# Performance work log

Measured on AMD Instinct MI355X. Metric: run time of the kernel, lower is better.

The kernel has to match this reference:

```python
import jax, jax.numpy as jnp
import numpy as np

N = 100000   # nodes per node type
E = 1000000  # edges per edge type
C = 128      # channels
H = 4        # num_heads
D = C // H   # head_dim


def setup_inputs() -> dict:
    key = jax.random.key(0)
    ks = jax.random.split(key, 16)
    return {
        "x_A": jax.random.normal(ks[0], (N, C), jnp.float32),
        "x_B": jax.random.normal(ks[1], (N, C), jnp.float32),
        "Wq": jax.random.normal(ks[2], (C, C), jnp.float32) * 0.05,
        "bq": jax.random.normal(ks[3], (C,), jnp.float32) * 0.05,
        "Wk": jax.random.normal(ks[4], (C, C), jnp.float32) * 0.05,
        "bk": jax.random.normal(ks[5], (C,), jnp.float32) * 0.05,
        "Wv": jax.random.normal(ks[6], (C, C), jnp.float32) * 0.05,
        "bv": jax.random.normal(ks[7], (C,), jnp.float32) * 0.05,
        "gamma": jnp.ones((C,), jnp.float32),
        "beta": jnp.zeros((C,), jnp.float32),
        "bias_AB": jax.random.normal(ks[8], (1,), jnp.float32),
        "bias_BA": jax.random.normal(ks[9], (1,), jnp.float32),
        "sb_AB": jax.random.normal(ks[10], (E,), jnp.float32),
        "sb_BA": jax.random.normal(ks[11], (E,), jnp.float32),
        "edge_index_AB": jax.random.randint(ks[12], (2, E), 0, N, jnp.int32),
        "edge_index_BA": jax.random.randint(ks[13], (2, E), 0, N, jnp.int32),
    }


def _edge_attention(x_src, x_dst, src, dst, sb, etype_bias, Wq, bq, Wk, bk, Wv, bv):
    """Per-edge-type attention: gather -> score -> dst-segment softmax -> scatter-add."""
    n_dst = x_dst.shape[0]
    Q = (x_dst @ Wq.T + bq).reshape(n_dst, H, D)
    K = (x_src @ Wk.T + bk).reshape(-1, H, D)
    V = (x_src @ Wv.T + bv).reshape(-1, H, D)
    # [E, H] per-edge scores
    scores = jnp.einsum('ehd,ehd->eh', Q[dst], K[src]) / np.float32(np.sqrt(D))
    scores = scores + sb[:, None] + etype_bias  # spatial bias + edge-type bias
    # segment softmax over edges grouped by dst node (numerically stable)
    m = jax.ops.segment_max(scores, dst, num_segments=n_dst)
    ex = jnp.exp(scores - m[dst])
    denom = jax.ops.segment_sum(ex, dst, num_segments=n_dst)
    w = ex / denom[dst]  # [E, H]
    msg = (V[src] * w[:, :, None]).reshape(-1, C)  # [E, C]
    return jax.ops.segment_sum(msg, dst, num_segments=n_dst)  # index_add_


def _layernorm(x, gamma, beta, eps=1e-5):
    mu = x.mean(-1, keepdims=True)
    var = ((x - mu) ** 2).mean(-1, keepdims=True)
    return (x - mu) / jnp.sqrt(var + eps) * gamma + beta


def _forward(x_A, x_B, Wq, bq, Wk, bk, Wv, bv, gamma, beta,
             bias_AB, bias_BA, sb_AB, sb_BA, edge_index_AB, edge_index_BA):
    src_ab, dst_ab = edge_index_AB[0], edge_index_AB[1]  # A -> B
    src_ba, dst_ba = edge_index_BA[0], edge_index_BA[1]  # B -> A
    lin = (Wq, bq, Wk, bk, Wv, bv)
    out_B = _edge_attention(x_A, x_B, src_ab, dst_ab, sb_AB, bias_AB, *lin)
    out_A = _edge_attention(x_B, x_A, src_ba, dst_ba, sb_BA, bias_BA, *lin)
    # total degree = in_deg + out_deg per node type
    ones_e = jnp.ones((E,), jnp.float32)
    deg_A = (jax.ops.segment_sum(ones_e, src_ab, num_segments=N)
             + jax.ops.segment_sum(ones_e, dst_ba, num_segments=N))
    deg_B = (jax.ops.segment_sum(ones_e, dst_ab, num_segments=N)
             + jax.ops.segment_sum(ones_e, src_ba, num_segments=N))
    out_A = out_A + deg_A[:, None]
    out_B = out_B + deg_B[:, None]
    out_A = _layernorm(out_A + x_A, gamma, beta)
    out_B = _layernorm(out_B + x_B, gamma, beta)
    return out_A, out_B


def reference(x_A, x_B, Wq, bq, Wk, bk, Wv, bv, gamma, beta,
              bias_AB, bias_BA, sb_AB, sb_BA, edge_index_AB, edge_index_BA):
    return _forward(x_A, x_B, Wq, bq, Wk, bk, Wv, bv, gamma, beta,
                    bias_AB, bias_BA, sb_AB, sb_BA, edge_index_AB, edge_index_BA)
```

## Files before the change

kernel.cpp:

```cpp
#include <hip/hip_runtime.h>

#define CH 128
#define QSCALE (0.17677669529663687f * 1.4426950408889634f)
#define LOG2E 1.4426950408889634f
#define SCAN_BLK 1024
#define KVSTRIDE 384

typedef _Float16 f16;
typedef _Float16 f16x2 __attribute__((ext_vector_type(2)));
typedef _Float16 f16x8 __attribute__((ext_vector_type(8)));
typedef __attribute__((ext_vector_type(4))) float f32x4;

__device__ __forceinline__ unsigned pk2(float a, float b) {
    auto h = __builtin_amdgcn_cvt_pkrtz(a, b);
    return __builtin_bit_cast(unsigned, h);
}
__device__ __forceinline__ f16x2 u2h(unsigned u) { return __builtin_bit_cast(f16x2, u); }

template <int CTRL>
__device__ __forceinline__ float dpp_add(float x) {
    const int t = __builtin_amdgcn_update_dpp(0, __builtin_bit_cast(int, x), CTRL, 0xF, 0xF, false);
    return x + __builtin_bit_cast(float, t);
}
__device__ __forceinline__ float head_sum(float x) {
    x = dpp_add<0xB1>(x);
    x = dpp_add<0x4E>(x);
    x = dpp_add<0x124>(x);
    x = dpp_add<0x128>(x);
    return x;
}

__global__ __launch_bounds__(256) void wcvt(const float* __restrict__ Wq, const float* __restrict__ Wk,
                                            const float* __restrict__ Wv, unsigned short* __restrict__ out)
{
    const int i = blockIdx.x * 256 + threadIdx.x;
    if (i >= 3 * CH * CH) return;
    const float* W = (i < CH * CH) ? Wq : (i < 2 * CH * CH) ? Wk : Wv;
    const float s = (i < CH * CH) ? QSCALE : 1.f;
    f16 h = (f16)(W[i & (CH * CH - 1)] * s);
    out[i] = __builtin_bit_cast(unsigned short, h);
}

__global__ __launch_bounds__(256) void qkv_mfma(
    const float* __restrict__ xA, const float* __restrict__ xB,
    const unsigned short* __restrict__ Wb,
    const float* __restrict__ bq, const float* __restrict__ bk, const float* __restrict__ bv,
    unsigned short* __restrict__ Qb,
    unsigned char* __restrict__ KVb,
    int n)
{
    __shared__ __align__(16) char lds[40960];
    const int type = blockIdx.y;
    const float* x = type ? xB : xA;
    const int bRow = blockIdx.x * 64;
    const int tid = threadIdx.x;

    #pragma unroll
    for (int j = 0; j < 8; ++j) {
        const int flat16 = j * 256 + tid;
        const int row = flat16 >> 5;
        const int c16 = flat16 & 31;
        float4 v = make_float4(0.f, 0.f, 0.f, 0.f);
        if (bRow + row < n) v = *(const float4*)(x + (size_t)(bRow + row) * CH + c16 * 4);
        const int off = (row * 256 + c16 * 8) ^ ((row & 7) << 4);
        *(uint2*)(lds + off) = make_uint2(pk2(v.x, v.y), pk2(v.z, v.w));
    }
    __syncthreads();

    const int w = tid >> 6, l = tid & 63, lr = l & 15, lg = l >> 4;
    const int colbase = w * 32;

    f32x4 acc[3][2][4];
    #pragma unroll
    for (int p = 0; p < 3; ++p)
        #pragma unroll
        for (int ct = 0; ct < 2; ++ct)
            #pragma unroll
            for (int rt = 0; rt < 4; ++rt)
                acc[p][ct][rt] = (f32x4){0.f, 0.f, 0.f, 0.f};

    #pragma unroll
    for (int kt = 0; kt < 4; ++kt) {
        f16x8 bx[4];
        #pragma unroll
        for (int rt = 0; rt < 4; ++rt) {
            const int row = rt * 16 + lr;
            const int off = (row * 256 + kt * 64 + lg * 16) ^ ((row & 7) << 4);
            bx[rt] = *(const f16x8*)(lds + off);
        }
        #pragma unroll
        for (int p = 0; p < 3; ++p) {
            #pragma unroll
            for (int ct = 0; ct < 2; ++ct) {
                const int ocol = colbase + ct * 16 + lr;
                const f16x8 a = *(const f16x8*)(Wb + ((size_t)p << 14) + (size_t)ocol * CH + kt * 32 + lg * 8);
                #pragma unroll
                for (int rt = 0; rt < 4; ++rt)
                    acc[p][ct][rt] = __builtin_amdgcn_mfma_f32_16x16x32_f16(a, bx[rt], acc[p][ct][rt], 0, 0, 0);
            }
        }
    }

    __syncthreads();

    #pragma unroll
    for (int ct = 0; ct < 2; ++ct) {
        const int c0 = colbase + ct * 16 + lg * 4;
        float4 bbq = *(const float4*)(bq + c0);
        bbq.x *= QSCALE; bbq.y *= QSCALE; bbq.z *= QSCALE; bbq.w *= QSCALE;
        const float4 bbk = *(const float4*)(bk + c0);
        const float4 bbv = *(const float4*)(bv + c0);
        const int cbq = w * 64 + ct * 32 + lg * 8;
        const int cbk = w * 32 + ct * 16 + lg * 4;
        #pragma unroll
        for (int rt = 0; rt < 4; ++rt) {
            const int nl = rt * 16 + lr;
            const int swz = (nl & 7) << 4;
            const f32x4 aq = acc[0][ct][rt], ak = acc[1][ct][rt], av = acc[2][ct][rt];
            *(uint2*)(lds + nl * 256 + (cbq ^ swz)) =
                make_uint2(pk2(aq[0] + bbq.x, aq[1] + bbq.y), pk2(aq[2] + bbq.z, aq[3] + bbq.w));
            int kw = __builtin_amdgcn_cvt_pk_fp8_f32(ak[0] + bbk.x, ak[1] + bbk.y, 0, false);
            kw     = __builtin_amdgcn_cvt_pk_fp8_f32(ak[2] + bbk.z, ak[3] + bbk.w, kw, true);
            *(unsigned*)(lds + 16384 + nl * 128 + (cbk ^ swz)) = (unsigned)kw;
            *(uint2*)(lds + 24576 + nl * 256 + (cbq ^ swz)) =
                make_uint2(pk2(av[0] + bbv.x, av[1] + bbv.y), pk2(av[2] + bbv.z, av[3] + bbv.w));
        }
    }
    __syncthreads();

    unsigned short* Qo = Qb + (size_t)type * n * CH;
    unsigned char* KVo = KVb + (size_t)type * n * KVSTRIDE;
    #pragma unroll
    for (int j = 0; j < 4; ++j) {
        const int flat = j * 256 + tid;
        const int row = flat >> 4, c16 = flat & 15;
        const uint4 val = *(const uint4*)(lds + row * 256 + ((c16 ^ (row & 7)) << 4));
        const int node = bRow + row;
        if (node < n) *(uint4*)(Qo + (size_t)node * CH + c16 * 8) = val;
    }
    #pragma unroll
    for (int j = 0; j < 2; ++j) {
        const int flat = j * 256 + tid;
        const int row = flat >> 3, c = flat & 7;
        const uint4 val = *(const uint4*)(lds + 16384 + row * 128 + ((c ^ (row & 7)) << 4));
        const int node = bRow + row;
        if (node < n) *(uint4*)(KVo + (size_t)node * KVSTRIDE + c * 16) = val;
    }
    #pragma unroll
    for (int j = 0; j < 4; ++j) {
        const int flat = j * 256 + tid;
        const int row = flat >> 4, c16 = flat & 15;
        const uint4 val = *(const uint4*)(lds + 24576 + row * 256 + ((c16 ^ (row & 7)) << 4));
        const int node = bRow + row;
        if (node < n) *(uint4*)(KVo + (size_t)node * KVSTRIDE + 128 + c16 * 16) = val;
    }
}

__global__ __launch_bounds__(256) void deg_hist(const int* __restrict__ eiAB, const int* __restrict__ eiBA,
                                                int* __restrict__ degAB, int* __restrict__ degBA,
                                                int nE, int ebl)
{
    const int dir = blockIdx.x >= ebl;
    const int e = ((blockIdx.x - dir * ebl) * 256 + threadIdx.x) * 4;
    if (e >= nE) return;
    const int* ei = dir ? eiBA : eiAB;
    int* deg = dir ? degBA : degAB;
    if (e + 3 < nE) {
        const int4 d4 = *(const int4*)(ei + nE + e);
        atomicAdd(&deg[d4.x], 1); atomicAdd(&deg[d4.y], 1);
        atomicAdd(&deg[d4.z], 1); atomicAdd(&deg[d4.w], 1);
    } else {
        for (int j = e; j < nE; ++j) atomicAdd(&deg[ei[nE + j]], 1);
    }
}

__global__ __launch_bounds__(256) void scan_local(const int* __restrict__ degAB, const int* __restrict__ degBA,
                                                  int* __restrict__ offsAB, int* __restrict__ offsBA,
                                                  int* __restrict__ bsums, int n, int nb)
{
    __shared__ int s[256];
    const int dir = blockIdx.x >= nb;
    const int blk = blockIdx.x - dir * nb;
    const int* deg = dir ? degBA : degAB;
    int* offs = dir ? offsBA : offsAB;
    int* bs = bsums + dir * 256;

    const int t = threadIdx.x;
    const int base = blk * SCAN_BLK + t * 4;
    int v0 = 0, v1 = 0, v2 = 0, v3 = 0;
    if (base + 3 < n) {
        int4 q = *(const int4*)(deg + base);
        v0 = q.x; v1 = q.y; v2 = q.z; v3 = q.w;
    } else {
        if (base + 0 < n) v0 = deg[base + 0];
        if (base + 1 < n) v1 = deg[base + 1];
        if (base + 2 < n) v2 = deg[base + 2];
    }
    const int tsum = v0 + v1 + v2 + v3;
    s[t] = tsum;
    __syncthreads();
    for (int off = 1; off < 256; off <<= 1) {
        int add = (t >= off) ? s[t - off] : 0;
        __syncthreads();
        s[t] += add;
        __syncthreads();
    }
    const int excl = s[t] - tsum;
    if (base + 0 < n) offs[base + 0] = excl;
    if (base + 1 < n) offs[base + 1] = excl + v0;
    if (base + 2 < n) offs[base + 2] = excl + v0 + v1;
    if (base + 3 < n) offs[base + 3] = excl + v0 + v1 + v2;
    if (t == 255) bs[blk] = s[255];
}

__global__ __launch_bounds__(256) void scan_bsums(int* __restrict__ bsums, int nb)
{
    __shared__ int s[256];
    int* bs = bsums + blockIdx.x * 256;
    const int t = threadIdx.x;
    int v = (t < nb) ? bs[t] : 0;
    s[t] = v;
    __syncthreads();
    for (int off = 1; off < 256; off <<= 1) {
        int add = (t >= off) ? s[t - off] : 0;
        __syncthreads();
        s[t] += add;
        __syncthreads();
    }
    if (t < nb) bs[t] = s[t] - v;
}

__global__ __launch_bounds__(256) void add_bsums(int* __restrict__ offsAB, int* __restrict__ offsBA,
                                                 int* __restrict__ curAB, int* __restrict__ curBA,
                                                 const int* __restrict__ bsums, int n, int nbl)
{
    const int dir = blockIdx.x >= nbl;
    const int i = (blockIdx.x - dir * nbl) * 256 + threadIdx.x;
    if (i >= n) return;
    int* offs = dir ? offsBA : offsAB;
    int* cur  = dir ? curBA  : curAB;
    const int v = offs[i] + bsums[dir * 256 + (i >> 10)];
    offs[i] = v;
    cur[i] = v;
}

__global__ __launch_bounds__(256) void csr_fill(const int* __restrict__ eiAB, const int* __restrict__ eiBA,
                                                const float* __restrict__ sbAB, const float* __restrict__ sbBA,
                                                const float* __restrict__ biasAB, const float* __restrict__ biasBA,
                                                int* __restrict__ curAB, int* __restrict__ curBA,
                                                int2* __restrict__ edAB, int2* __restrict__ edBA,
                                                int nE, int ebl)
{
    const int dir = blockIdx.x >= ebl;
    const int e = ((blockIdx.x - dir * ebl) * 256 + threadIdx.x) * 4;
    if (e >= nE) return;
    const int* ei = dir ? eiBA : eiAB;
    const float* sb = dir ? sbBA : sbAB;
    const float bia = dir ? biasBA[0] : biasAB[0];
    int* cur = dir ? curBA : curAB;
    int2* ed = dir ? edBA : edAB;
    if (e + 3 < nE) {
        const int4 s4 = *(const int4*)(ei + e);
        const int4 d4 = *(const int4*)(ei + nE + e);
        const float4 b4 = *(const float4*)(sb + e);
        int p0 = atomicAdd(&cur[d4.x], 1); ed[p0] = make_int2(s4.x, __float_as_int((b4.x + bia) * LOG2E));
        int p1 = atomicAdd(&cur[d4.y], 1); ed[p1] = make_int2(s4.y, __float_as_int((b4.y + bia) * LOG2E));
        int p2 = atomicAdd(&cur[d4.z], 1); ed[p2] = make_int2(s4.z, __float_as_int((b4.z + bia) * LOG2E));
        int p3 = atomicAdd(&cur[d4.w], 1); ed[p3] = make_int2(s4.w, __float_as_int((b4.w + bia) * LOG2E));
    } else {
        for (int j = e; j < nE; ++j) {
            const int pos = atomicAdd(&cur[ei[nE + j]], 1);
            ed[pos] = make_int2(ei[j], __float_as_int((sb[j] + bia) * LOG2E));
        }
    }
}

__global__ __launch_bounds__(256) void attn_node(
    const unsigned short* __restrict__ Qb,
    const unsigned char* __restrict__ KVb,
    const float* __restrict__ xA, const float* __restrict__ xB,
    const int* __restrict__ offsAB, const int* __restrict__ offsBA,
    const int* __restrict__ degAB, const int* __restrict__ degBA,
    const int2* __restrict__ edAB, const int2* __restrict__ edBA,
    const float* __restrict__ gamma, const float* __restrict__ beta,
    float* __restrict__ out, int n, int abl)
{
    const int dir = blockIdx.x >= abl;
    const int node = (blockIdx.x - dir * abl) * 4 + (threadIdx.x >> 6);
    if (node >= n) return;
    const int l = threadIdx.x & 63;
    const int l2 = l * 2;

    const unsigned short* Q = Qb + (size_t)dir * n * CH;
    const unsigned char* KV = KVb + (size_t)(1 - dir) * n * KVSTRIDE;
    const float* x = dir ? xB : xA;
    const int* offs = dir ? offsAB : offsBA;
    const int* deg  = dir ? degAB  : degBA;
    const int2* ed  = dir ? edAB   : edBA;
    float* o = out + (size_t)dir * n * CH;

    const f16x2 qp = u2h(*(const unsigned*)(Q + (size_t)node * CH + l2));
    const float qf0 = (float)qp[0], qf1 = (float)qp[1];

    const int beg = __builtin_amdgcn_readfirstlane(offs[node]);
    const int d   = __builtin_amdgcn_readfirstlane(deg[node]);

    float m = -3.0e38f, den = 0.f;
    f16x2 a01 = (f16x2){(f16)0.f, (f16)0.f};

    auto loadE = [&](int i, float& sbf, unsigned& kc, unsigned& vc) {
        if (i < d) {
            const int2 e = ed[beg + i];
            sbf = __int_as_float(e.y);
            const unsigned b = (unsigned)e.x * (unsigned)KVSTRIDE;
            kc = *(const unsigned short*)(KV + b + l2);
            vc = *(const unsigned*)(KV + b + 128 + l2 * 2);
        } else {
            sbf = __int_as_float((int)0xFF800000u);
            kc = 0; vc = 0;
        }
    };

    auto procPair = [&](float sf0, unsigned k0, unsigned v0,
                        float sf1, unsigned k1, unsigned v1) {
        const auto kf0 = __builtin_amdgcn_cvt_pk_f32_fp8((int)k0, false);
        const auto kf1 = __builtin_amdgcn_cvt_pk_f32_fp8((int)k1, false);
        float sa = head_sum(fmaf(qf0, kf0[0], qf1 * kf0[1])) + sf0;
        float sb = head_sum(fmaf(qf0, kf1[0], qf1 * kf1[1])) + sf1;
        const float pm = fmaxf(sa, sb);
        if (!__all(pm <= m + 8.f)) {
            const float mn = fmaxf(m, pm);
            const float sc = exp2f(m - mn);
            den *= sc;
            a01 *= u2h(pk2(sc, sc));
            m = mn;
        }
        const float ea = exp2f(sa - m);
        const float eb = exp2f(sb - m);
        den += ea + eb;
        a01 += u2h(pk2(ea, ea)) * u2h(v0);
        a01 += u2h(pk2(eb, eb)) * u2h(v1);
    };

    float sA0, sA1, sA2, sA3, sB0, sB1, sB2, sB3;
    unsigned kA0, kA1, kA2, kA3, kB0, kB1, kB2, kB3;
    unsigned vA0, vA1, vA2, vA3, vB0, vB1, vB2, vB3;
    loadE(0, sA0, kA0, vA0); loadE(1, sA1, kA1, vA1);
    loadE(2, sA2, kA2, vA2); loadE(3, sA3, kA3, vA3);
    loadE(4, sB0, kB0, vB0); loadE(5, sB1, kB1, vB1);
    loadE(6, sB2, kB2, vB2); loadE(7, sB3, kB3, vB3);

    for (int i = 0; i < d; i += 8) {
        procPair(sA0, kA0, vA0, sA1, kA1, vA1);
        procPair(sA2, kA2, vA2, sA3, kA3, vA3);
        loadE(i + 8,  sA0, kA0, vA0); loadE(i + 9,  sA1, kA1, vA1);
        loadE(i + 10, sA2, kA2, vA2); loadE(i + 11, sA3, kA3, vA3);
        procPair(sB0, kB0, vB0, sB1, kB1, vB1);
        procPair(sB2, kB2, vB2, sB3, kB3, vB3);
        loadE(i + 12, sB0, kB0, vB0); loadE(i + 13, sB1, kB1, vB1);
        loadE(i + 14, sB2, kB2, vB2); loadE(i + 15, sB3, kB3, vB3);
    }

    const float inv = (den > 0.f) ? 1.f / den : 0.f;
    const float2 xv = *(const float2*)(x + (size_t)node * CH + l2);
    const float w0 = (float)a01[0] * inv + xv.x;
    const float w1 = (float)a01[1] * inv + xv.y;

    float sum = w0 + w1;
    #pragma unroll
    for (int off = 32; off; off >>= 1) sum += __shfl_xor(sum, off);
    const float mean = sum * (1.f / 128.f);
    const float c0 = w0 - mean, c1 = w1 - mean;
    float vs = c0 * c0 + c1 * c1;
    #pragma unroll
    for (int off = 32; off; off >>= 1) vs += __shfl_xor(vs, off);
    const float rstd = rsqrtf(vs * (1.f / 128.f) + 1e-5f);

    const float2 g = *(const float2*)(gamma + l2);
    const float2 bt = *(const float2*)(beta + l2);
    float2 ov;
    ov.x = c0 * rstd * g.x + bt.x;
    ov.y = c1 * rstd * g.y + bt.y;
    *(float2*)(o + (size_t)node * CH + l2) = ov;
}

extern "C" void kernel_launch(void* const* d_in, const int* in_sizes, int n_in,
                              void* d_out, int out_size, void* d_ws, size_t ws_size,
                              hipStream_t stream)
{
    const float* xA     = (const float*)d_in[0];
    const float* xB     = (const float*)d_in[1];
    const float* Wq     = (const float*)d_in[2];
    const float* bq     = (const float*)d_in[3];
    const float* Wk     = (const float*)d_in[4];
    const float* bk     = (const float*)d_in[5];
    const float* Wv     = (const float*)d_in[6];
    const float* bv     = (const float*)d_in[7];
    const float* gamma  = (const float*)d_in[8];
    const float* beta   = (const float*)d_in[9];
    const float* biasAB = (const float*)d_in[10];
    const float* biasBA = (const float*)d_in[11];
    const float* sbAB   = (const float*)d_in[12];
    const float* sbBA   = (const float*)d_in[13];
    const int*   eiAB   = (const int*)d_in[14];
    const int*   eiBA   = (const int*)d_in[15];

    const int n  = in_sizes[0] / CH;
    const int nE = in_sizes[12];
    const size_t NC = (size_t)n * CH;

    char* p = (char*)d_ws;
    auto carve = [&](size_t bytes) { char* r = p; p += (bytes + 15) & ~(size_t)15; return r; };
    unsigned short* Qb = (unsigned short*)carve(2 * NC * 2);
    unsigned char*  KVb = (unsigned char*)carve((size_t)2 * n * KVSTRIDE);
    unsigned short* Wb  = (unsigned short*)carve(3 * CH * CH * 2);
    int2* edAB  = (int2*)carve((size_t)nE * 8);
    int2* edBA  = (int2*)carve((size_t)nE * 8);
    int* offsAB = (int*)carve((size_t)n * 4);
    int* offsBA = (int*)carve((size_t)n * 4);
    int* degAB  = (int*)carve((size_t)2 * n * 4);
    int* degBA  = degAB + n;
    int* curAB  = (int*)carve((size_t)n * 4);
    int* curBA  = (int*)carve((size_t)n * 4);
    int* bsums  = (int*)carve(2 * 256 * 4);

    float* out = (float*)d_out;

    (void)hipMemsetAsync(degAB, 0, (size_t)2 * n * sizeof(int), stream);

    wcvt<<<(3 * CH * CH + 255) / 256, 256, 0, stream>>>(Wq, Wk, Wv, Wb);

    dim3 qkv_grid((n + 63) / 64, 2);
    qkv_mfma<<<qkv_grid, 256, 0, stream>>>(xA, xB, Wb, bq, bk, bv, Qb, KVb, n);

    const int ebl4 = (nE + 1023) / 1024;
    deg_hist<<<2 * ebl4, 256, 0, stream>>>(eiAB, eiBA, degAB, degBA, nE, ebl4);

    const int nb = (n + SCAN_BLK - 1) / SCAN_BLK;
    scan_local<<<2 * nb, 256, 0, stream>>>(degAB, degBA, offsAB, offsBA, bsums, n, nb);
    scan_bsums<<<2, 256, 0, stream>>>(bsums, nb);
    const int nbl = (n + 255) / 256;
    add_bsums<<<2 * nbl, 256, 0, stream>>>(offsAB, offsBA, curAB, curBA, bsums, n, nbl);

    csr_fill<<<2 * ebl4, 256, 0, stream>>>(eiAB, eiBA, sbAB, sbBA, biasAB, biasBA,
                                           curAB, curBA, edAB, edBA, nE, ebl4);

    const int abl = (n + 3) / 4;
    attn_node<<<2 * abl, 256, 0, stream>>>(Qb, KVb, xA, xB, offsAB, offsBA, degAB, degBA,
                                           edAB, edBA, gamma, beta, out, n, abl);
}
```

Baseline: 488.7 us.

## Shrink QKV LDS staging, fold block-sum scan into add kernel, prescale edge offsets

The QKV epilogue now stages Q, K and V through one 16KB LDS buffer in three passes instead of a 40KB buffer, which allows more resident blocks per CU at the cost of extra barriers. The separate scan_bsums launch is removed: every add_bsums block rescans the small block-sum array in shared memory itself. csr_fill stores source indices premultiplied by the KV row stride, saving a multiply per edge in the attention kernel. deg_hist is also launched before the QKV GEMM.

```diff
diff --git a/kernel.cpp b/kernel.cpp
--- a/kernel.cpp
+++ b/kernel.cpp
@@ -49,7 +49,7 @@
     unsigned char* __restrict__ KVb,
     int n)
 {
-    __shared__ __align__(16) char lds[40960];
+    __shared__ __align__(16) char lds[16384];
     const int type = blockIdx.y;
     const float* x = type ? xB : xA;
     const int bRow = blockIdx.x * 64;
@@ -101,58 +101,58 @@
         }
     }
 
-    __syncthreads();
-
-    #pragma unroll
-    for (int ct = 0; ct < 2; ++ct) {
-        const int c0 = colbase + ct * 16 + lg * 4;
-        float4 bbq = *(const float4*)(bq + c0);
-        bbq.x *= QSCALE; bbq.y *= QSCALE; bbq.z *= QSCALE; bbq.w *= QSCALE;
-        const float4 bbk = *(const float4*)(bk + c0);
-        const float4 bbv = *(const float4*)(bv + c0);
-        const int cbq = w * 64 + ct * 32 + lg * 8;
-        const int cbk = w * 32 + ct * 16 + lg * 4;
-        #pragma unroll
-        for (int rt = 0; rt < 4; ++rt) {
-            const int nl = rt * 16 + lr;
-            const int swz = (nl & 7) << 4;
-            const f32x4 aq = acc[0][ct][rt], ak = acc[1][ct][rt], av = acc[2][ct][rt];
-            *(uint2*)(lds + nl * 256 + (cbq ^ swz)) =
-                make_uint2(pk2(aq[0] + bbq.x, aq[1] + bbq.y), pk2(aq[2] + bbq.z, aq[3] + bbq.w));
-            int kw = __builtin_amdgcn_cvt_pk_fp8_f32(ak[0] + bbk.x, ak[1] + bbk.y, 0, false);
-            kw     = __builtin_amdgcn_cvt_pk_fp8_f32(ak[2] + bbk.z, ak[3] + bbk.w, kw, true);
-            *(unsigned*)(lds + 16384 + nl * 128 + (cbk ^ swz)) = (unsigned)kw;
-            *(uint2*)(lds + 24576 + nl * 256 + (cbq ^ swz)) =
-                make_uint2(pk2(av[0] + bbv.x, av[1] + bbv.y), pk2(av[2] + bbv.z, av[3] + bbv.w));
-        }
-    }
-    __syncthreads();
-
     unsigned short* Qo = Qb + (size_t)type * n * CH;
     unsigned char* KVo = KVb + (size_t)type * n * KVSTRIDE;
-    #pragma unroll
-    for (int j = 0; j < 4; ++j) {
-        const int flat = j * 256 + tid;
-        const int row = flat >> 4, c16 = flat & 15;
-        const uint4 val = *(const uint4*)(lds + row * 256 + ((c16 ^ (row & 7)) << 4));
-        const int node = bRow + row;
-        if (node < n) *(uint4*)(Qo + (size_t)node * CH + c16 * 8) = val;
-    }
-    #pragma unroll
-    for (int j = 0; j < 2; ++j) {
-        const int flat = j * 256 + tid;
-        const int row = flat >> 3, c = flat & 7;
-        const uint4 val = *(const uint4*)(lds + 16384 + row * 128 + ((c ^ (row & 7)) << 4));
-        const int node = bRow + row;
-        if (node < n) *(uint4*)(KVo + (size_t)node * KVSTRIDE + c * 16) = val;
-    }
-    #pragma unroll
-    for (int j = 0; j < 4; ++j) {
-        const int flat = j * 256 + tid;
-        const int row = flat >> 4, c16 = flat & 15;
-        const uint4 val = *(const uint4*)(lds + 24576 + row * 256 + ((c16 ^ (row & 7)) << 4));
-        const int node = bRow + row;
-        if (node < n) *(uint4*)(KVo + (size_t)node * KVSTRIDE + 128 + c16 * 16) = val;
+
+    #pragma unroll
+    for (int p = 0; p < 3; ++p) {
+        __syncthreads();
+        const float* bias = (p == 0) ? bq : (p == 1) ? bk : bv;
+        #pragma unroll
+        for (int ct = 0; ct < 2; ++ct) {
+            const int c0 = colbase + ct * 16 + lg * 4;
+            float4 bb = *(const float4*)(bias + c0);
+            if (p == 0) { bb.x *= QSCALE; bb.y *= QSCALE; bb.z *= QSCALE; bb.w *= QSCALE; }
+            #pragma unroll
+            for (int rt = 0; rt < 4; ++rt) {
+                const int nl = rt * 16 + lr;
+                const int swz = (nl & 7) << 4;
+                const f32x4 a4 = acc[p][ct][rt];
+                if (p == 1) {
+                    const int cbk = w * 32 + ct * 16 + lg * 4;
+                    int kw = __builtin_amdgcn_cvt_pk_fp8_f32(a4[0] + bb.x, a4[1] + bb.y, 0, false);
+                    kw     = __builtin_amdgcn_cvt_pk_fp8_f32(a4[2] + bb.z, a4[3] + bb.w, kw, true);
+                    *(unsigned*)(lds + nl * 128 + (cbk ^ swz)) = (unsigned)kw;
+                } else {
+                    const int cbq = w * 64 + ct * 32 + lg * 8;
+                    *(uint2*)(lds + nl * 256 + (cbq ^ swz)) =
+                        make_uint2(pk2(a4[0] + bb.x, a4[1] + bb.y), pk2(a4[2] + bb.z, a4[3] + bb.w));
+                }
+            }
+        }
+        __syncthreads();
+        if (p == 1) {
+            #pragma unroll
+            for (int j = 0; j < 2; ++j) {
+                const int flat = j * 256 + tid;
+                const int row = flat >> 3, c = flat & 7;
+                const uint4 val = *(const uint4*)(lds + row * 128 + ((c ^ (row & 7)) << 4));
+                const int node = bRow + row;
+                if (node < n) *(uint4*)(KVo + (size_t)node * KVSTRIDE + c * 16) = val;
+            }
+        } else {
+            #pragma unroll
+            for (int j = 0; j < 4; ++j) {
+                const int flat = j * 256 + tid;
+                const int row = flat >> 4, c16 = flat & 15;
+                const uint4 val = *(const uint4*)(lds + row * 256 + ((c16 ^ (row & 7)) << 4));
+                const int node = bRow + row;
+                if (node < n) {
+                    if (p == 0) *(uint4*)(Qo + (size_t)node * CH + c16 * 8) = val;
+                    else        *(uint4*)(KVo + (size_t)node * KVSTRIDE + 128 + c16 * 16) = val;
+                }
+            }
+        }
     }
 }
 
@@ -213,12 +213,15 @@
     if (t == 255) bs[blk] = s[255];
 }
 
-__global__ __launch_bounds__(256) void scan_bsums(int* __restrict__ bsums, int nb)
+__global__ __launch_bounds__(256) void add_bsums(int* __restrict__ offsAB, int* __restrict__ offsBA,
+                                                 int* __restrict__ curAB, int* __restrict__ curBA,
+                                                 const int* __restrict__ bsums, int n, int nbl, int nb)
 {
     __shared__ int s[256];
-    int* bs = bsums + blockIdx.x * 256;
+    const int dir = blockIdx.x >= nbl;
+    const int blk = blockIdx.x - dir * nbl;
     const int t = threadIdx.x;
-    int v = (t < nb) ? bs[t] : 0;
+    int v = (t < nb) ? bsums[dir * 256 + t] : 0;
     s[t] = v;
     __syncthreads();
     for (int off = 1; off < 256; off <<= 1) {
@@ -227,21 +230,15 @@
         s[t] += add;
         __syncthreads();
     }
-    if (t < nb) bs[t] = s[t] - v;
-}
-
-__global__ __launch_bounds__(256) void add_bsums(int* __restrict__ offsAB, int* __restrict__ offsBA,
-                                                 int* __restrict__ curAB, int* __restrict__ curBA,
-                                                 const int* __restrict__ bsums, int n, int nbl)
-{
-    const int dir = blockIdx.x >= nbl;
-    const int i = (blockIdx.x - dir * nbl) * 256 + threadIdx.x;
+    const int i = blk * 256 + t;
     if (i >= n) return;
+    const int bi = i >> 10;
+    const int excl = (bi == 0) ? 0 : s[bi - 1];
     int* offs = dir ? offsBA : offsAB;
     int* cur  = dir ? curBA  : curAB;
-    const int v = offs[i] + bsums[dir * 256 + (i >> 10)];
-    offs[i] = v;
-    cur[i] = v;
+    const int vv = offs[i] + excl;
+    offs[i] = vv;
+    cur[i] = vv;
 }
 
 __global__ __launch_bounds__(256) void csr_fill(const int* __restrict__ eiAB, const int* __restrict__ eiBA,
@@ -263,14 +260,14 @@
         const int4 s4 = *(const int4*)(ei + e);
         const int4 d4 = *(const int4*)(ei + nE + e);
         const float4 b4 = *(const float4*)(sb + e);
-        int p0 = atomicAdd(&cur[d4.x], 1); ed[p0] = make_int2(s4.x, __float_as_int((b4.x + bia) * LOG2E));
-        int p1 = atomicAdd(&cur[d4.y], 1); ed[p1] = make_int2(s4.y, __float_as_int((b4.y + bia) * LOG2E));
-        int p2 = atomicAdd(&cur[d4.z], 1); ed[p2] = make_int2(s4.z, __float_as_int((b4.z + bia) * LOG2E));
-        int p3 = atomicAdd(&cur[d4.w], 1); ed[p3] = make_int2(s4.w, __float_as_int((b4.w + bia) * LOG2E));
+        int p0 = atomicAdd(&cur[d4.x], 1); ed[p0] = make_int2(s4.x * KVSTRIDE, __float_as_int((b4.x + bia) * LOG2E));
+        int p1 = atomicAdd(&cur[d4.y], 1); ed[p1] = make_int2(s4.y * KVSTRIDE, __float_as_int((b4.y + bia) * LOG2E));
+        int p2 = atomicAdd(&cur[d4.z], 1); ed[p2] = make_int2(s4.z * KVSTRIDE, __float_as_int((b4.z + bia) * LOG2E));
+        int p3 = atomicAdd(&cur[d4.w], 1); ed[p3] = make_int2(s4.w * KVSTRIDE, __float_as_int((b4.w + bia) * LOG2E));
     } else {
         for (int j = e; j < nE; ++j) {
             const int pos = atomicAdd(&cur[ei[nE + j]], 1);
-            ed[pos] = make_int2(ei[j], __float_as_int((sb[j] + bia) * LOG2E));
+            ed[pos] = make_int2(ei[j] * KVSTRIDE, __float_as_int((sb[j] + bia) * LOG2E));
         }
     }
 }
@@ -312,7 +309,7 @@
         if (i < d) {
             const int2 e = ed[beg + i];
             sbf = __int_as_float(e.y);
-            const unsigned b = (unsigned)e.x * (unsigned)KVSTRIDE;
+            const unsigned b = (unsigned)e.x;
             kc = *(const unsigned short*)(KV + b + l2);
             vc = *(const unsigned*)(KV + b + 128 + l2 * 2);
         } else {
@@ -430,17 +427,16 @@
 
     wcvt<<<(3 * CH * CH + 255) / 256, 256, 0, stream>>>(Wq, Wk, Wv, Wb);
 
+    const int ebl4 = (nE + 1023) / 1024;
+    deg_hist<<<2 * ebl4, 256, 0, stream>>>(eiAB, eiBA, degAB, degBA, nE, ebl4);
+
     dim3 qkv_grid((n + 63) / 64, 2);
     qkv_mfma<<<qkv_grid, 256, 0, stream>>>(xA, xB, Wb, bq, bk, bv, Qb, KVb, n);
 
-    const int ebl4 = (nE + 1023) / 1024;
-    deg_hist<<<2 * ebl4, 256, 0, stream>>>(eiAB, eiBA, degAB, degBA, nE, ebl4);
-
     const int nb = (n + SCAN_BLK - 1) / SCAN_BLK;
     scan_local<<<2 * nb, 256, 0, stream>>>(degAB, degBA, offsAB, offsBA, bsums, n, nb);
-    scan_bsums<<<2, 256, 0, stream>>>(bsums, nb);
     const int nbl = (n + 255) / 256;
-    add_bsums<<<2 * nbl, 256, 0, stream>>>(offsAB, offsBA, curAB, curBA, bsums, n, nbl);
+    add_bsums<<<2 * nbl, 256, 0, stream>>>(offsAB, offsBA, curAB, curBA, bsums, n, nbl, nb);
 
     csr_fill<<<2 * ebl4, 256, 0, stream>>>(eiAB, eiBA, sbAB, sbBA, biasAB, biasBA,
                                            curAB, curBA, edAB, edBA, nE, ebl4);
```

Result: slower. 501.8 us (+2.7%).
